# Kernel optimization log

Measured on AMD Instinct MI355X. Metric: run time of the kernel, lower is better.

The kernel has to match this reference:

```python
import jax, jax.numpy as jnp
import numpy as np

# ---- db4 filters (pywt conventions: dec_lo = rec_lo[::-1], rec_hi = qmf(rec_lo)) ----
F = 8  # db4 filter length
_rec_lo = np.array([0.23037781330885523, 0.7148465705525415, 0.6308807679295904,
                    -0.027983769416983849, -0.18703481171888114, 0.030841381835986965,
                    0.032883011666982945, -0.010597401784997278], dtype=np.float32)
_rec_hi = _rec_lo[::-1].copy()
_rec_hi[1::2] *= -1.0
REC_LO = jnp.asarray(_rec_lo)
REC_HI = jnp.asarray(_rec_hi)

MAX_LEVEL = 9  # pywt.dwt_max_level(4096, 8)


def _conv1d(x, kernel, stride=1, padding='VALID', lhs_dilation=None):
    # x: [B, L] -> correlation (XLA conv does NOT flip the kernel)
    out = jax.lax.conv_general_dilated(
        x[:, None, :], kernel[None, None, :],
        window_strides=(stride,), padding=padding,
        lhs_dilation=lhs_dilation,
        dimension_numbers=('NCH', 'OIH', 'NCH'))
    return out[:, 0, :]


def dwt(x):
    # pywt.dwt(x, 'db4', mode='symmetric'):
    # cA = np.convolve(sym_ext(x, F-1), dec_lo, 'valid')[1::2]
    # convolution with dec filter == correlation with rec filter (its reverse)
    ext = jnp.pad(x, ((0, 0), (F - 1, F - 1)), mode='symmetric')[:, 1:]
    return _conv1d(ext, REC_LO, stride=2), _conv1d(ext, REC_HI, stride=2)


def idwt(ca, cd):
    # pywt.idwt: zero-upsample coeffs, full convolution with rec filters, trim edges
    n = ca.shape[1]
    pad = ((F - 1, F - 1),)
    out = (_conv1d(ca, REC_LO[::-1], padding=pad, lhs_dilation=(2,)) +
           _conv1d(cd, REC_HI[::-1], padding=pad, lhs_dilation=(2,)))
    return out[:, F - 2:2 * n]  # output length = 2n - F + 2


def wavelet_features(x1):
    # Faithful to WaveletDWTLayer stack + WaveletParsingLayer: at each level k>=2,
    # reconstruct with details of levels k and k-1 only (others zeroed), with
    # pywt.waverec's trim-by-one rule; concatenate the 8 full-length reconstructions.
    a = x1
    cds, recs = [], []
    for level in range(1, MAX_LEVEL + 1):
        a, d = dwt(a)
        if level >= 2:
            r = idwt(jnp.zeros_like(d), d)
            for j in range(level - 2, -1, -1):
                dj = cds[j] if j == level - 2 else jnp.zeros_like(cds[j])
                if r.shape[1] == dj.shape[1] + 1:  # waverec trim rule
                    r = r[:, :-1]
                r = idwt(r, dj)
            recs.append(r)  # [B, signal_length]
        cds.append(d)
    return jnp.concatenate(recs, axis=1)  # [B, signal_length*(MAX_LEVEL-1)]


def reference(x1, x2, x3, W0, b0, W1, b1, W2, b2):
    # x2/x3 are placeholders in the original module (overwritten by layers 1/2)
    h = wavelet_features(x1)
    for W, b in ((W0, b0), (W1, b1), (W2, b2)):
        h = jax.nn.relu(h) @ W.T + b
    return h


def setup_inputs() -> dict:
    key = jax.random.key(0)
    ks = jax.random.split(key, 4)
    B, N = 2048, 4096
    D_IN, H1, H2, OUT = 32768, 181, 13, 10
    return {
        'x1': jax.random.normal(ks[0], (B, N), jnp.float32),
        'x2': jnp.zeros((B, 1, 8), jnp.float32),
        'x3': jnp.zeros((B, 1, 8), jnp.float32),
        'W0': jax.random.normal(ks[1], (H1, D_IN), jnp.float32) / np.float32(np.sqrt(D_IN)),
        'b0': jnp.zeros((H1,), jnp.float32),
        'W1': jax.random.normal(ks[2], (H2, H1), jnp.float32) / np.float32(np.sqrt(H1)),
        'b1': jnp.zeros((H2,), jnp.float32),
        'W2': jax.random.normal(ks[3], (OUT, H2), jnp.float32) / np.float32(np.sqrt(H2)),
        'b2': jnp.zeros((OUT,), jnp.float32),
    }
```

## Files before the change

kernel.cpp:

```cpp
#include <hip/hip_runtime.h>
#include <hip/hip_bf16.h>


typedef _Float16 f16x8 __attribute__((ext_vector_type(8)));
typedef _Float16 f16x4v __attribute__((ext_vector_type(4)));
typedef float f32x4 __attribute__((ext_vector_type(4)));

#define WV_THREADS 256
#define DROW 4160
#define NSPLIT 32
#define KCHUNK 1024
#define GEMM_BM 256

#define L0 0.23037781330885523f
#define L1 0.7148465705525415f
#define L2f 0.6308807679295904f
#define L3 -0.02798376941698385f
#define L4 -0.18703481171888114f
#define L5 0.030841381835986965f
#define L6 0.032883011666982945f
#define L7 -0.010597401784997278f

#define H0 -0.010597401784997278f
#define H1 -0.032883011666982945f
#define H2 0.030841381835986965f
#define H3 0.18703481171888114f
#define H4 -0.02798376941698385f
#define H5 -0.6308807679295904f
#define H6 0.7148465705525415f
#define H7 -0.23037781330885523f

__constant__ constexpr int cNL[10]   = {4096, 2051, 1029, 518, 262, 134, 70, 38, 22, 14};
__constant__ constexpr int cDOFF[10] = {0, 0, 2052, 3084, 3604, 3868, 4004, 4076, 4116, 4140};

__device__ __forceinline__ int ext_idx(int j, int n) {
  return (j < 6) ? (5 - j) : ((j < n + 6) ? (j - 6) : (2 * n + 5 - j));
}

__device__ __forceinline__ void dwt2(const float* a, float* anext, float* d,
                                     int n, int m, bool store_a) {
  const int ng = (m + 1) >> 1;
  for (int g = threadIdx.x; g < ng; g += WV_THREADS) {
    float w[10];
    if (g >= 2 && 4 * g + 9 <= n + 5) {
      const float2* af = (const float2*)a + (2 * g - 3);
      float2 b0 = af[0], b1 = af[1], b2 = af[2], b3 = af[3], b4 = af[4];
      w[0] = b0.x; w[1] = b0.y; w[2] = b1.x; w[3] = b1.y; w[4] = b2.x;
      w[5] = b2.y; w[6] = b3.x; w[7] = b3.y; w[8] = b4.x; w[9] = b4.y;
    } else {
#pragma unroll
      for (int q = 0; q < 10; ++q) {
        int j = 4 * g + q;
        int jm = n + 12;
        if (j > jm) j = jm;
        w[q] = a[ext_idx(j, n)];
      }
    }
    float sl0 = w[0]*L0 + w[1]*L1 + w[2]*L2f + w[3]*L3 + w[4]*L4 + w[5]*L5 + w[6]*L6 + w[7]*L7;
    float sh0 = w[0]*H0 + w[1]*H1 + w[2]*H2  + w[3]*H3 + w[4]*H4 + w[5]*H5 + w[6]*H6 + w[7]*H7;
    float sl1 = w[2]*L0 + w[3]*L1 + w[4]*L2f + w[5]*L3 + w[6]*L4 + w[7]*L5 + w[8]*L6 + w[9]*L7;
    float sh1 = w[2]*H0 + w[3]*H1 + w[4]*H2  + w[5]*H3 + w[6]*H4 + w[7]*H5 + w[8]*H6 + w[9]*H7;
    if (2 * g + 1 < m) {
      if (store_a) *(float2*)(anext + 2 * g) = make_float2(sl0, sl1);
      *(float2*)(d + 2 * g) = make_float2(sh0, sh1);
    } else {
      if (store_a) anext[2 * g] = sl0;
      d[2 * g] = sh0;
    }
  }
}

#define SWZ(u) ((u) ^ (((u) >> 3) & 7))
__device__ __forceinline__ const float4* lds4c(const float* b, int s) {
  return (const float4*)b + SWZ(s);
}
__device__ __forceinline__ float4* lds4(float* b, int s) {
  return (float4*)b + SWZ(s);
}

template <bool HAS_CA, bool HAS_CD, bool FINAL, int N>
__device__ __forceinline__ void step16(const float* ca, const float* cd,
                                       float* outl, _Float16* outg) {
  constexpr int npair = N - 3;
  constexpr int ng = (npair + 7) >> 3;
  const int t = threadIdx.x;
  if (t >= ng) return;
  float w[12], v[12];
  if constexpr (HAS_CA) {
    float4 a = *lds4c(ca, 2 * t), b = *lds4c(ca, 2 * t + 1), c = *lds4c(ca, 2 * t + 2);
    w[0]=a.x; w[1]=a.y; w[2]=a.z; w[3]=a.w; w[4]=b.x; w[5]=b.y; w[6]=b.z; w[7]=b.w;
    w[8]=c.x; w[9]=c.y; w[10]=c.z; w[11]=c.w;
  }
  if constexpr (HAS_CD) {
    const float4* p = (const float4*)(cd + 8 * t);
    float4 a = p[0], b = p[1], c = p[2];
    v[0]=a.x; v[1]=a.y; v[2]=a.z; v[3]=a.w; v[4]=b.x; v[5]=b.y; v[6]=b.z; v[7]=b.w;
    v[8]=c.x; v[9]=c.y; v[10]=c.z; v[11]=c.w;
  }
  float E[8], O[8];
#pragma unroll
  for (int pp = 0; pp < 8; ++pp) {
    float e = 0.f, o = 0.f;
    if constexpr (HAS_CA) {
      e = w[pp+3]*L0 + w[pp+2]*L2f + w[pp+1]*L4 + w[pp]*L6;
      o = w[pp+3]*L1 + w[pp+2]*L3  + w[pp+1]*L5 + w[pp]*L7;
    }
    if constexpr (HAS_CD) {
      e += v[pp+3]*H0 + v[pp+2]*H2 + v[pp+1]*H4 + v[pp]*H6;
      o += v[pp+3]*H1 + v[pp+2]*H3 + v[pp+1]*H5 + v[pp]*H7;
    }
    E[pp] = e; O[pp] = o;
  }
  if constexpr (FINAL) {
    f16x8 h0, h1;
    h0[0]=(_Float16)fmaxf(E[0],0.f); h0[1]=(_Float16)fmaxf(O[0],0.f);
    h0[2]=(_Float16)fmaxf(E[1],0.f); h0[3]=(_Float16)fmaxf(O[1],0.f);
    h0[4]=(_Float16)fmaxf(E[2],0.f); h0[5]=(_Float16)fmaxf(O[2],0.f);
    h0[6]=(_Float16)fmaxf(E[3],0.f); h0[7]=(_Float16)fmaxf(O[3],0.f);
    h1[0]=(_Float16)fmaxf(E[4],0.f); h1[1]=(_Float16)fmaxf(O[4],0.f);
    h1[2]=(_Float16)fmaxf(E[5],0.f); h1[3]=(_Float16)fmaxf(O[5],0.f);
    h1[4]=(_Float16)fmaxf(E[6],0.f); h1[5]=(_Float16)fmaxf(O[6],0.f);
    h1[6]=(_Float16)fmaxf(E[7],0.f); h1[7]=(_Float16)fmaxf(O[7],0.f);
    *(f16x8*)(outg + 16 * t) = h0;
    *(f16x8*)(outg + 16 * t + 8) = h1;
  } else {
#pragma unroll
    for (int j = 0; j < 4; ++j) {
      const int p2 = 8 * t + 2 * j;
      if (p2 + 1 < npair) {
        *lds4(outl, 4 * t + j) = make_float4(E[2*j], O[2*j], E[2*j+1], O[2*j+1]);
      } else if (p2 < npair) {
        *(float2*)lds4(outl, 4 * t + j) = make_float2(E[2*j], O[2*j]);
      }
    }
  }
}

__device__ __forceinline__ void nocd2_core(const float w[12], float r[11],
                                           float E[8], float O[8]) {
#pragma unroll
  for (int h = 0; h < 6; ++h) {
    float e = w[h+3]*L0 + w[h+2]*L2f + w[h+1]*L4 + w[h]*L6;
    float o = w[h+3]*L1 + w[h+2]*L3  + w[h+1]*L5 + w[h]*L7;
    r[2*h] = e;
    if (2*h + 1 < 11) r[2*h+1] = o;
  }
#pragma unroll
  for (int pp = 0; pp < 8; ++pp) {
    E[pp] = r[pp+3]*L0 + r[pp+2]*L2f + r[pp+1]*L4 + r[pp]*L6;
    O[pp] = r[pp+3]*L1 + r[pp+2]*L3  + r[pp+1]*L5 + r[pp]*L7;
  }
}

template <int N1>
__device__ __forceinline__ void pair16(const float* cur, float* outl) {
  constexpr int N2 = (2 * N1 - 6 == 1030) ? 1029 : (2 * N1 - 6);
  constexpr int np2 = N2 - 3;
  constexpr int ng = (np2 + 7) >> 3;
  const int t = threadIdx.x;
  if (t >= ng) return;
  float w[12];
  float4 a = *lds4c(cur, t), b = *lds4c(cur, t + 1), c = *lds4c(cur, t + 2);
  w[0]=a.x; w[1]=a.y; w[2]=a.z; w[3]=a.w; w[4]=b.x; w[5]=b.y; w[6]=b.z; w[7]=b.w;
  w[8]=c.x; w[9]=c.y; w[10]=c.z; w[11]=c.w;
  float r[11], E[8], O[8];
  nocd2_core(w, r, E, O);
#pragma unroll
  for (int j = 0; j < 4; ++j) {
    const int p2 = 8 * t + 2 * j;
    if (p2 + 1 < np2) {
      *lds4(outl, 4 * t + j) = make_float4(E[2*j], O[2*j], E[2*j+1], O[2*j+1]);
    } else if (p2 < np2) {
      *(float2*)lds4(outl, 4 * t + j) = make_float2(E[2*j], O[2*j]);
    }
  }
}

__device__ __forceinline__ void finpair16(const float* cur, _Float16* outg) {
  const int t = threadIdx.x;
  float w[12];
  float4 a = *lds4c(cur, t), b = *lds4c(cur, t + 1), c = *lds4c(cur, t + 2);
  w[0]=a.x; w[1]=a.y; w[2]=a.z; w[3]=a.w; w[4]=b.x; w[5]=b.y; w[6]=b.z; w[7]=b.w;
  w[8]=c.x; w[9]=c.y; w[10]=c.z; w[11]=c.w;
  float r[11], E[8], O[8];
  nocd2_core(w, r, E, O);
  f16x8 h0, h1;
  h0[0]=(_Float16)fmaxf(E[0],0.f); h0[1]=(_Float16)fmaxf(O[0],0.f);
  h0[2]=(_Float16)fmaxf(E[1],0.f); h0[3]=(_Float16)fmaxf(O[1],0.f);
  h0[4]=(_Float16)fmaxf(E[2],0.f); h0[5]=(_Float16)fmaxf(O[2],0.f);
  h0[6]=(_Float16)fmaxf(E[3],0.f); h0[7]=(_Float16)fmaxf(O[3],0.f);
  h1[0]=(_Float16)fmaxf(E[4],0.f); h1[1]=(_Float16)fmaxf(O[4],0.f);
  h1[2]=(_Float16)fmaxf(E[5],0.f); h1[3]=(_Float16)fmaxf(O[5],0.f);
  h1[4]=(_Float16)fmaxf(E[6],0.f); h1[5]=(_Float16)fmaxf(O[6],0.f);
  h1[6]=(_Float16)fmaxf(E[7],0.f); h1[7]=(_Float16)fmaxf(O[7],0.f);
  *(f16x8*)(outg + 16 * t) = h0;
  *(f16x8*)(outg + 16 * t + 8) = h1;
}

template <int NL, int NLm1>
__device__ __forceinline__ void initpair16(const float* cdL, const float* cdm,
                                           float* outl) {
  constexpr int np2 = NLm1 - 3;
  constexpr int ng = (np2 + 7) >> 3;
  const int t = threadIdx.x;
  if (t >= ng) return;
  float w[12];
  {
    const float4* p = (const float4*)(cdL + 4 * t);
    float4 a = p[0], b = p[1], c = p[2];
    w[0]=a.x; w[1]=a.y; w[2]=a.z; w[3]=a.w; w[4]=b.x; w[5]=b.y; w[6]=b.z; w[7]=b.w;
    w[8]=c.x; w[9]=c.y; w[10]=c.z; w[11]=c.w;
  }
  float r[11];
#pragma unroll
  for (int h = 0; h < 6; ++h) {
    float e = w[h+3]*H0 + w[h+2]*H2 + w[h+1]*H4 + w[h]*H6;
    float o = w[h+3]*H1 + w[h+2]*H3 + w[h+1]*H5 + w[h]*H7;
    r[2*h] = e;
    if (2*h + 1 < 11) r[2*h+1] = o;
  }
  float v[12];
  {
    const float4* p = (const float4*)(cdm + 8 * t);
    float4 a = p[0], b = p[1], c = p[2];
    v[0]=a.x; v[1]=a.y; v[2]=a.z; v[3]=a.w; v[4]=b.x; v[5]=b.y; v[6]=b.z; v[7]=b.w;
    v[8]=c.x; v[9]=c.y; v[10]=c.z; v[11]=c.w;
  }
  float E[8], O[8];
#pragma unroll
  for (int pp = 0; pp < 8; ++pp) {
    E[pp] = r[pp+3]*L0 + r[pp+2]*L2f + r[pp+1]*L4 + r[pp]*L6
          + v[pp+3]*H0 + v[pp+2]*H2  + v[pp+1]*H4 + v[pp]*H6;
    O[pp] = r[pp+3]*L1 + r[pp+2]*L3  + r[pp+1]*L5 + r[pp]*L7
          + v[pp+3]*H1 + v[pp+2]*H3  + v[pp+1]*H5 + v[pp]*H7;
  }
#pragma unroll
  for (int j = 0; j < 4; ++j) {
    const int p2 = 8 * t + 2 * j;
    if (p2 + 1 < np2) {
      *lds4(outl, 4 * t + j) = make_float4(E[2*j], O[2*j], E[2*j+1], O[2*j+1]);
    } else if (p2 < np2) {
      *(float2*)lds4(outl, 4 * t + j) = make_float2(E[2*j], O[2*j]);
    }
  }
}

template <int L>
__device__ __forceinline__ void synth2(const float* dr, _Float16* og,
                                       float* s1, float* s2) {
  if constexpr (L == 2) {
    step16<false, true, false, 1029>(nullptr, dr + cDOFF[2], s1, nullptr);
    __syncthreads();
    step16<true, true, true, 2051>(s1, dr + cDOFF[1], nullptr, og);
  } else {
    initpair16<cNL[L], cNL[L - 1]>(dr + cDOFF[L], dr + cDOFF[L - 1], s1);
    __syncthreads();
    if constexpr (L == 3) {
      step16<true, false, true, 2051>(s1, nullptr, nullptr, og);
    } else if constexpr (L == 4) {
      finpair16(s1, og);
    } else if constexpr (L == 5) {
      pair16<518>(s1, s2); __syncthreads();
      step16<true, false, true, 2051>(s2, nullptr, nullptr, og);
    } else if constexpr (L == 6) {
      pair16<262>(s1, s2); __syncthreads();
      finpair16(s2, og);
    } else if constexpr (L == 7) {
      pair16<134>(s1, s2); __syncthreads();
      pair16<518>(s2, s1); __syncthreads();
      step16<true, false, true, 2051>(s1, nullptr, nullptr, og);
    } else if constexpr (L == 8) {
      pair16<70>(s1, s2); __syncthreads();
      pair16<262>(s2, s1); __syncthreads();
      finpair16(s1, og);
    } else {
      pair16<38>(s1, s2); __syncthreads();
      pair16<134>(s2, s1); __syncthreads();
      pair16<518>(s1, s2); __syncthreads();
      step16<true, false, true, 2051>(s2, nullptr, nullptr, og);
    }
  }
}

__global__ __launch_bounds__(WV_THREADS) void wv_analysis_cvt(
    const float* __restrict__ x, float* __restrict__ dG,
    const float* __restrict__ W0, _Float16* __restrict__ Bw) {
  __shared__ float r1[4104];
  __shared__ float r2[2056];
  const int tid = threadIdx.x;

  if (blockIdx.x >= 2048) {
    size_t i = ((size_t)(blockIdx.x - 2048) * 256 + tid) * 4;
    int rowc = (int)(i >> 15);
    f16x4v h;
    if (rowc < 181) {
      const float4 v = *(const float4*)(W0 + i);
      h[0] = (_Float16)v.x; h[1] = (_Float16)v.y;
      h[2] = (_Float16)v.z; h[3] = (_Float16)v.w;
    } else {
      h[0] = (_Float16)0.f; h[1] = (_Float16)0.f;
      h[2] = (_Float16)0.f; h[3] = (_Float16)0.f;
    }
    *(f16x4v*)(Bw + i) = h;
    return;
  }

  const int NLa[10]  = {4096, 2051, 1029, 518, 262, 134, 70, 38, 22, 14};
  const int DOFF[10] = {0, 0, 2052, 3084, 3604, 3868, 4004, 4076, 4116, 4140};
  const int LOFF[10] = {0, 0, 1036, 520, 2068, 1040, 2332, 1176, 2404, 1216};
  const int row = blockIdx.x;

  const float4* xr = (const float4*)(x + (size_t)row * 4096);
  for (int i = tid; i < 1024; i += WV_THREADS) ((float4*)r1)[i] = xr[i];
  __syncthreads();

  float* dr = dG + (size_t)row * DROW;
  dwt2(r1, r2, dr + DOFF[1], NLa[0], NLa[1], true);
  __syncthreads();
  const float* ap = r2;
  float* an = r1;
  for (int lev = 2; lev <= 9; ++lev) {
    float* dbuf = ((lev & 1) ? r2 : r1) + LOFF[lev];
    dwt2(ap, an, dbuf, NLa[lev - 1], NLa[lev], lev < 9);
    __syncthreads();
    const float* t = ap; ap = an; an = (float*)t;
  }
  for (int lev = 2; lev <= 9; ++lev) {
    const float* src = ((lev & 1) ? r2 : r1) + LOFF[lev];
    float* dst = dr + DOFF[lev];
    const int n = NLa[lev];
    for (int i = 2 * tid; i + 1 < n; i += 2 * WV_THREADS)
      *(float2*)(dst + i) = *(const float2*)(src + i);
    if ((n & 1) && tid == 0) dst[n - 1] = src[n - 1];
  }
}

__global__ __launch_bounds__(WV_THREADS, 8) void wv_synth(
    const float* __restrict__ dG, _Float16* __restrict__ A) {
  __shared__ alignas(16) float s1[2080];
  __shared__ alignas(16) float s2[2080];
  const int row = blockIdx.x;
  const float* dr = dG + (size_t)row * DROW;
  _Float16* og = A + (size_t)row * 32768 + (size_t)blockIdx.y * 4096;
  switch (blockIdx.y) {
    case 0: synth2<2>(dr, og, s1, s2); break;
    case 1: synth2<3>(dr, og, s1, s2); break;
    case 2: synth2<4>(dr, og, s1, s2); break;
    case 3: synth2<5>(dr, og, s1, s2); break;
    case 4: synth2<6>(dr, og, s1, s2); break;
    case 5: synth2<7>(dr, og, s1, s2); break;
    case 6: synth2<8>(dr, og, s1, s2); break;
    default: synth2<9>(dr, og, s1, s2); break;
  }
}

__device__ __forceinline__ void load_lds16(const void* g, void* l) {
  __builtin_amdgcn_global_load_lds((__attribute__((address_space(1))) unsigned int*)g,
                                   (__attribute__((address_space(3))) unsigned int*)l,
                                   16, 0, 0);
}

__global__ __launch_bounds__(512, 2) void gemm_kernel(
    const _Float16* __restrict__ A, const _Float16* __restrict__ Bw,
    float* __restrict__ P) {
  __shared__ _Float16 As[2][GEMM_BM * 64];
  __shared__ _Float16 Bs[2][192 * 64];
  const int tid = threadIdx.x;
  const int lane = tid & 63;
  const int wave = tid >> 6;
  const int m0 = blockIdx.x * GEMM_BM;
  const int k_idx = blockIdx.y;
  const int k0 = k_idx * KCHUNK;

  f32x4 acc[2][12];
#pragma unroll
  for (int mt = 0; mt < 2; ++mt)
#pragma unroll
    for (int nt = 0; nt < 12; ++nt) acc[mt][nt] = (f32x4){0.f, 0.f, 0.f, 0.f};

  auto stage = [&](int ks, int b) {
    const int kbase = k0 + (ks << 6);
#pragma unroll
    for (int t = 0; t < 4; ++t) {
      int c = wave * 4 + t;
      int g = (c << 6) + lane;
      int r = g >> 3, cs = g & 7;
      const _Float16* gp = A + (size_t)(m0 + r) * 32768 + kbase + ((cs ^ (r & 7)) << 3);
      load_lds16(gp, (char*)As[b] + ((size_t)c << 10));
    }
#pragma unroll
    for (int t = 0; t < 3; ++t) {
      int c = wave * 3 + t;
      int g = (c << 6) + lane;
      int r = g >> 3, cs = g & 7;
      const _Float16* gp = Bw + (size_t)r * 32768 + kbase + ((cs ^ (r & 7)) << 3);
      load_lds16(gp, (char*)Bs[b] + ((size_t)c << 10));
    }
  };

  stage(0, 0);
  __syncthreads();

  for (int ks = 0; ks < (KCHUNK >> 6); ++ks) {
    const int cur = ks & 1;
    if (ks + 1 < (KCHUNK >> 6)) stage(ks + 1, cur ^ 1);
#pragma unroll
    for (int kk = 0; kk < 2; ++kk) {
      const int chunk = kk * 4 + (lane >> 4);
      f16x8 af[2];
#pragma unroll
      for (int mt = 0; mt < 2; ++mt) {
        int r = wave * 32 + mt * 16 + (lane & 15);
        af[mt] = *(const f16x8*)(As[cur] + r * 64 + ((chunk ^ (r & 7)) << 3));
      }
#pragma unroll
      for (int nt = 0; nt < 12; ++nt) {
        int rb = nt * 16 + (lane & 15);
        f16x8 bf = *(const f16x8*)(Bs[cur] + rb * 64 + ((chunk ^ (rb & 7)) << 3));
        acc[0][nt] = __builtin_amdgcn_mfma_f32_16x16x32_f16(af[0], bf, acc[0][nt], 0, 0, 0);
        acc[1][nt] = __builtin_amdgcn_mfma_f32_16x16x32_f16(af[1], bf, acc[1][nt], 0, 0, 0);
      }
    }
    __syncthreads();
  }

  float* Pp = P + ((size_t)k_idx * 2048 + m0) * 192;
#pragma unroll
  for (int mt = 0; mt < 2; ++mt)
#pragma unroll
    for (int nt = 0; nt < 12; ++nt)
#pragma unroll
      for (int r4 = 0; r4 < 4; ++r4) {
        int rr = wave * 32 + mt * 16 + ((lane >> 4) << 2) + r4;
        int cc = nt * 16 + (lane & 15);
        Pp[(size_t)rr * 192 + cc] = acc[mt][nt][r4];
      }
}

__global__ __launch_bounds__(256) void mlp_kernel(
    const float* __restrict__ P, const float* __restrict__ b0,
    const float* __restrict__ W1, const float* __restrict__ b1,
    const float* __restrict__ W2, const float* __restrict__ b2,
    float* __restrict__ out) {
  __shared__ float part[4][193];
  __shared__ float h1[192];
  __shared__ float h2[13];
  const int row = blockIdx.x;
  const int t = threadIdx.x;
  const int g = t >> 6;
  const int l = t & 63;

  float a0 = 0.f, a1 = 0.f, a2 = 0.f;
  for (int si = 0; si < NSPLIT / 4; ++si) {
    int s = g + (si << 2);
    const float* Pr = P + ((size_t)s * 2048 + row) * 192;
    a0 += Pr[l]; a1 += Pr[64 + l]; a2 += Pr[128 + l];
  }
  part[g][l] = a0; part[g][64 + l] = a1; part[g][128 + l] = a2;
  __syncthreads();

  if (t < 192) {
    float v = part[0][t] + part[1][t] + part[2][t] + part[3][t];
    h1[t] = (t < 181) ? fmaxf(v + b0[t], 0.f) : 0.f;
  }
  __syncthreads();

#pragma unroll
  for (int r = 0; r < 4; ++r) {
    int j = g + (r << 2);
    if (j < 13) {
      float v = 0.f;
#pragma unroll
      for (int q = 0; q < 3; ++q) {
        int n = l + (q << 6);
        if (n < 181) v += h1[n] * W1[j * 181 + n];
      }
      for (int off = 32; off >= 1; off >>= 1) v += __shfl_down(v, off);
      if (l == 0) h2[j] = fmaxf(v + b1[j], 0.f);
    }
  }
  __syncthreads();

  if (t < 10) {
    float c = b2[t];
#pragma unroll
    for (int j = 0; j < 13; ++j) c += h2[j] * W2[t * 13 + j];
    out[(size_t)row * 10 + t] = c;
  }
}

extern "C" void kernel_launch(void* const* d_in, const int* in_sizes, int n_in,
                              void* d_out, int out_size, void* d_ws, size_t ws_size,
                              hipStream_t stream) {
  const float* x1 = (const float*)d_in[0];
  const float* W0 = (const float*)d_in[3];
  const float* b0 = (const float*)d_in[4];
  const float* W1 = (const float*)d_in[5];
  const float* b1 = (const float*)d_in[6];
  const float* W2 = (const float*)d_in[7];
  const float* b2 = (const float*)d_in[8];
  float* out = (float*)d_out;

  char* ws = (char*)d_ws;
  const size_t A_BYTES = (size_t)2048 * 32768 * 2;
  const size_t B_BYTES = (size_t)192 * 32768 * 2;
  _Float16* Afeat = (_Float16*)ws;
  _Float16* Bw = (_Float16*)(ws + A_BYTES);
  float* Dq = (float*)(ws + A_BYTES + B_BYTES);
  float* P = (float*)(ws + A_BYTES + B_BYTES);

  wv_analysis_cvt<<<2048 + 6144, WV_THREADS, 0, stream>>>(x1, Dq, W0, Bw);
  dim3 sg(2048, 8);
  wv_synth<<<sg, WV_THREADS, 0, stream>>>(Dq, Afeat);
  dim3 gg(2048 / GEMM_BM, NSPLIT);
  gemm_kernel<<<gg, 512, 0, stream>>>(Afeat, Bw, P);
  mlp_kernel<<<2048, 256, 0, stream>>>(P, b0, W1, b1, W2, b2, out);
}
```

Baseline: 224.0 us.

## Fuse short wavelet synthesis levels in registers and pipeline GEMM loads with vmcnt waits

For levels 2-4 the synthesis now runs the whole short reconstruction chain in registers per thread (fin2/fin3/fin4), reading detail coefficients straight from global memory. This removes the LDS round trips and barriers those levels used before. The GEMM main loop is restructured to issue the next stage's global-to-LDS loads and then wait only on the older loads (vmcnt(7)) with raw s_barrier, so loads overlap the MFMA compute. This relies on the count of outstanding loads per stage being exactly 7 for correctness.

Result: no change. 222.1 us (-0.9%).

```diff
diff --git a/kernel.cpp b/kernel.cpp
--- a/kernel.cpp
+++ b/kernel.cpp
@@ -78,6 +78,90 @@
   return (float4*)b + SWZ(s);
 }
 
+template <int NP>
+__device__ __forceinline__ void lvlL(const float* a, float* v) {
+#pragma unroll
+  for (int q = 0; q < NP; ++q) {
+    v[2*q]   = a[q+3]*L0 + a[q+2]*L2f + a[q+1]*L4 + a[q]*L6;
+    v[2*q+1] = a[q+3]*L1 + a[q+2]*L3  + a[q+1]*L5 + a[q]*L7;
+  }
+}
+template <int NP>
+__device__ __forceinline__ void lvlH(const float* d, float* v) {
+#pragma unroll
+  for (int q = 0; q < NP; ++q) {
+    v[2*q]   = d[q+3]*H0 + d[q+2]*H2 + d[q+1]*H4 + d[q]*H6;
+    v[2*q+1] = d[q+3]*H1 + d[q+2]*H3 + d[q+1]*H5 + d[q]*H7;
+  }
+}
+template <int NP>
+__device__ __forceinline__ void lvlLH(const float* a, const float* d, float* v) {
+#pragma unroll
+  for (int q = 0; q < NP; ++q) {
+    v[2*q]   = a[q+3]*L0 + a[q+2]*L2f + a[q+1]*L4 + a[q]*L6
+             + d[q+3]*H0 + d[q+2]*H2  + d[q+1]*H4 + d[q]*H6;
+    v[2*q+1] = a[q+3]*L1 + a[q+2]*L3  + a[q+1]*L5 + a[q]*L7
+             + d[q+3]*H1 + d[q+2]*H3  + d[q+1]*H5 + d[q]*H7;
+  }
+}
+
+__device__ __forceinline__ void g8f2(const float* p, int s, float* w) {
+#pragma unroll
+  for (int i = 0; i < 4; ++i) {
+    float2 v = *(const float2*)(p + s + 2 * i);
+    w[2*i] = v.x; w[2*i+1] = v.y;
+  }
+}
+__device__ __forceinline__ void g12f4(const float* p, int s, float* w) {
+#pragma unroll
+  for (int i = 0; i < 3; ++i) {
+    float4 v = *(const float4*)(p + s + 4 * i);
+    w[4*i] = v.x; w[4*i+1] = v.y; w[4*i+2] = v.z; w[4*i+3] = v.w;
+  }
+}
+
+__device__ __forceinline__ void store16(_Float16* outg, int t, const float* v) {
+  f16x8 h0, h1;
+#pragma unroll
+  for (int i = 0; i < 8; ++i) h0[i] = (_Float16)fmaxf(v[i], 0.f);
+#pragma unroll
+  for (int i = 0; i < 8; ++i) h1[i] = (_Float16)fmaxf(v[8 + i], 0.f);
+  *(f16x8*)(outg + 16 * t) = h0;
+  *(f16x8*)(outg + 16 * t + 8) = h1;
+}
+
+__device__ __forceinline__ void fin2(const float* d2, const float* d1, _Float16* og) {
+  const int t = threadIdx.x;
+  float dw[12];  g12f4(d2, 4 * t, dw);
+  float mid[12]; lvlH<6>(dw, mid);
+  float d1w[12]; g12f4(d1, 8 * t, d1w);
+  float v[16];   lvlLH<8>(mid, d1w, v);
+  store16(og, t, v);
+}
+
+__device__ __forceinline__ void fin3(const float* d3, const float* d2, _Float16* og) {
+  const int t = threadIdx.x;
+  float dw[8];   g8f2(d3, 2 * t, dw);
+  float v0[10];  lvlH<5>(dw, v0);
+  float d2w[12]; g12f4(d2, 4 * t, d2w);
+  float v1[12];  lvlLH<6>(v0, d2w, v1);
+  float v[16];   lvlL<8>(v1, v);
+  store16(og, t, v);
+}
+
+__device__ __forceinline__ void fin4(const float* d4, const float* d3, _Float16* og) {
+  const int t = threadIdx.x;
+  float dw[7];
+#pragma unroll
+  for (int i = 0; i < 7; ++i) dw[i] = d4[t + i];
+  float v0[8];   lvlH<4>(dw, v0);
+  float d3w[8];  g8f2(d3, 2 * t, d3w);
+  float v1[10];  lvlLH<5>(v0, d3w, v1);
+  float v2[12];  lvlL<6>(v1, v2);
+  float v[16];   lvlL<8>(v2, v);
+  store16(og, t, v);
+}
+
 template <bool HAS_CA, bool HAS_CD, bool FINAL, int N>
 __device__ __forceinline__ void step16(const float* ca, const float* cd,
                                        float* outl, _Float16* outg) {
@@ -112,17 +196,10 @@
     E[pp] = e; O[pp] = o;
   }
   if constexpr (FINAL) {
-    f16x8 h0, h1;
-    h0[0]=(_Float16)fmaxf(E[0],0.f); h0[1]=(_Float16)fmaxf(O[0],0.f);
-    h0[2]=(_Float16)fmaxf(E[1],0.f); h0[3]=(_Float16)fmaxf(O[1],0.f);
-    h0[4]=(_Float16)fmaxf(E[2],0.f); h0[5]=(_Float16)fmaxf(O[2],0.f);
-    h0[6]=(_Float16)fmaxf(E[3],0.f); h0[7]=(_Float16)fmaxf(O[3],0.f);
-    h1[0]=(_Float16)fmaxf(E[4],0.f); h1[1]=(_Float16)fmaxf(O[4],0.f);
-    h1[2]=(_Float16)fmaxf(E[5],0.f); h1[3]=(_Float16)fmaxf(O[5],0.f);
-    h1[4]=(_Float16)fmaxf(E[6],0.f); h1[5]=(_Float16)fmaxf(O[6],0.f);
-    h1[6]=(_Float16)fmaxf(E[7],0.f); h1[7]=(_Float16)fmaxf(O[7],0.f);
-    *(f16x8*)(outg + 16 * t) = h0;
-    *(f16x8*)(outg + 16 * t + 8) = h1;
+    float vv[16];
+#pragma unroll
+    for (int q = 0; q < 8; ++q) { vv[2*q] = E[q]; vv[2*q+1] = O[q]; }
+    store16(outg, t, vv);
   } else {
 #pragma unroll
     for (int j = 0; j < 4; ++j) {
@@ -184,17 +261,10 @@
   w[8]=c.x; w[9]=c.y; w[10]=c.z; w[11]=c.w;
   float r[11], E[8], O[8];
   nocd2_core(w, r, E, O);
-  f16x8 h0, h1;
-  h0[0]=(_Float16)fmaxf(E[0],0.f); h0[1]=(_Float16)fmaxf(O[0],0.f);
-  h0[2]=(_Float16)fmaxf(E[1],0.f); h0[3]=(_Float16)fmaxf(O[1],0.f);
-  h0[4]=(_Float16)fmaxf(E[2],0.f); h0[5]=(_Float16)fmaxf(O[2],0.f);
-  h0[6]=(_Float16)fmaxf(E[3],0.f); h0[7]=(_Float16)fmaxf(O[3],0.f);
-  h1[0]=(_Float16)fmaxf(E[4],0.f); h1[1]=(_Float16)fmaxf(O[4],0.f);
-  h1[2]=(_Float16)fmaxf(E[5],0.f); h1[3]=(_Float16)fmaxf(O[5],0.f);
-  h1[4]=(_Float16)fmaxf(E[6],0.f); h1[5]=(_Float16)fmaxf(O[6],0.f);
-  h1[6]=(_Float16)fmaxf(E[7],0.f); h1[7]=(_Float16)fmaxf(O[7],0.f);
-  *(f16x8*)(outg + 16 * t) = h0;
-  *(f16x8*)(outg + 16 * t + 8) = h1;
+  float vv[16];
+#pragma unroll
+  for (int q = 0; q < 8; ++q) { vv[2*q] = E[q]; vv[2*q+1] = O[q]; }
+  store16(outg, t, vv);
 }
 
 template <int NL, int NLm1>
@@ -241,43 +311,6 @@
       *lds4(outl, 4 * t + j) = make_float4(E[2*j], O[2*j], E[2*j+1], O[2*j+1]);
     } else if (p2 < np2) {
       *(float2*)lds4(outl, 4 * t + j) = make_float2(E[2*j], O[2*j]);
-    }
-  }
-}
-
-template <int L>
-__device__ __forceinline__ void synth2(const float* dr, _Float16* og,
-                                       float* s1, float* s2) {
-  if constexpr (L == 2) {
-    step16<false, true, false, 1029>(nullptr, dr + cDOFF[2], s1, nullptr);
-    __syncthreads();
-    step16<true, true, true, 2051>(s1, dr + cDOFF[1], nullptr, og);
-  } else {
-    initpair16<cNL[L], cNL[L - 1]>(dr + cDOFF[L], dr + cDOFF[L - 1], s1);
-    __syncthreads();
-    if constexpr (L == 3) {
-      step16<true, false, true, 2051>(s1, nullptr, nullptr, og);
-    } else if constexpr (L == 4) {
-      finpair16(s1, og);
-    } else if constexpr (L == 5) {
-      pair16<518>(s1, s2); __syncthreads();
-      step16<true, false, true, 2051>(s2, nullptr, nullptr, og);
-    } else if constexpr (L == 6) {
-      pair16<262>(s1, s2); __syncthreads();
-      finpair16(s2, og);
-    } else if constexpr (L == 7) {
-      pair16<134>(s1, s2); __syncthreads();
-      pair16<518>(s2, s1); __syncthreads();
-      step16<true, false, true, 2051>(s1, nullptr, nullptr, og);
-    } else if constexpr (L == 8) {
-      pair16<70>(s1, s2); __syncthreads();
-      pair16<262>(s2, s1); __syncthreads();
-      finpair16(s1, og);
-    } else {
-      pair16<38>(s1, s2); __syncthreads();
-      pair16<134>(s2, s1); __syncthreads();
-      pair16<518>(s1, s2); __syncthreads();
-      step16<true, false, true, 2051>(s2, nullptr, nullptr, og);
     }
   }
 }
@@ -343,14 +376,43 @@
   const float* dr = dG + (size_t)row * DROW;
   _Float16* og = A + (size_t)row * 32768 + (size_t)blockIdx.y * 4096;
   switch (blockIdx.y) {
-    case 0: synth2<2>(dr, og, s1, s2); break;
-    case 1: synth2<3>(dr, og, s1, s2); break;
-    case 2: synth2<4>(dr, og, s1, s2); break;
-    case 3: synth2<5>(dr, og, s1, s2); break;
-    case 4: synth2<6>(dr, og, s1, s2); break;
-    case 5: synth2<7>(dr, og, s1, s2); break;
-    case 6: synth2<8>(dr, og, s1, s2); break;
-    default: synth2<9>(dr, og, s1, s2); break;
+    case 0: fin2(dr + cDOFF[2], dr + cDOFF[1], og); break;
+    case 1: fin3(dr + cDOFF[3], dr + cDOFF[2], og); break;
+    case 2: fin4(dr + cDOFF[4], dr + cDOFF[3], og); break;
+    case 3:
+      initpair16<cNL[5], cNL[4]>(dr + cDOFF[5], dr + cDOFF[4], s1);
+      __syncthreads();
+      pair16<518>(s1, s2); __syncthreads();
+      step16<true, false, true, 2051>(s2, nullptr, nullptr, og);
+      break;
+    case 4:
+      initpair16<cNL[6], cNL[5]>(dr + cDOFF[6], dr + cDOFF[5], s1);
+      __syncthreads();
+      pair16<262>(s1, s2); __syncthreads();
+      finpair16(s2, og);
+      break;
+    case 5:
+      initpair16<cNL[7], cNL[6]>(dr + cDOFF[7], dr + cDOFF[6], s1);
+      __syncthreads();
+      pair16<134>(s1, s2); __syncthreads();
+      pair16<518>(s2, s1); __syncthreads();
+      step16<true, false, true, 2051>(s1, nullptr, nullptr, og);
+      break;
+    case 6:
+      initpair16<cNL[8], cNL[7]>(dr + cDOFF[8], dr + cDOFF[7], s1);
+      __syncthreads();
+      pair16<70>(s1, s2); __syncthreads();
+      pair16<262>(s2, s1); __syncthreads();
+      finpair16(s1, og);
+      break;
+    default:
+      initpair16<cNL[9], cNL[8]>(dr + cDOFF[9], dr + cDOFF[8], s1);
+      __syncthreads();
+      pair16<38>(s1, s2); __syncthreads();
+      pair16<134>(s2, s1); __syncthreads();
+      pair16<518>(s1, s2); __syncthreads();
+      step16<true, false, true, 2051>(s2, nullptr, nullptr, og);
+      break;
   }
 }
 
@@ -398,12 +460,7 @@
     }
   };
 
-  stage(0, 0);
-  __syncthreads();
-
-  for (int ks = 0; ks < (KCHUNK >> 6); ++ks) {
-    const int cur = ks & 1;
-    if (ks + 1 < (KCHUNK >> 6)) stage(ks + 1, cur ^ 1);
+  auto compute = [&](int cur) {
 #pragma unroll
     for (int kk = 0; kk < 2; ++kk) {
       const int chunk = kk * 4 + (lane >> 4);
@@ -421,8 +478,20 @@
         acc[1][nt] = __builtin_amdgcn_mfma_f32_16x16x32_f16(af[1], bf, acc[1][nt], 0, 0, 0);
       }
     }
-    __syncthreads();
-  }
+  };
+
+  constexpr int NT = KCHUNK >> 6;
+  stage(0, 0);
+  for (int ks = 0; ks < NT - 1; ++ks) {
+    stage(ks + 1, (ks + 1) & 1);
+    asm volatile("s_waitcnt vmcnt(7)" ::: "memory");
+    __builtin_amdgcn_s_barrier();
+    compute(ks & 1);
+    __builtin_amdgcn_s_barrier();
+  }
+  asm volatile("s_waitcnt vmcnt(0)" ::: "memory");
+  __builtin_amdgcn_s_barrier();
+  compute((NT - 1) & 1);
 
   float* Pp = P + ((size_t)k_idx * 2048 + m0) * 192;
 #pragma unroll
```
